# Optimization experiments

Hardware: AMD Instinct MI355X
Metric: run time of the kernel (lower is better)

## Reference

```python
import jax, jax.numpy as jnp
import numpy as np
from jax import lax


def _conv1d(x, w):
    # x: (B, L, C), w: (K, C, C), SAME padding (flax nnx.Conv default)
    return lax.conv_general_dilated(x, w, (1,), 'SAME', dimension_numbers=('NWC', 'WIO', 'NWC'))


def _message_passing(x, w, vertical, reverse):
    # x: (B, H, W, C). Sequential SCNN update along H (vertical) or W (horizontal):
    #   slice_i += relu(conv1d(slice_{i-1}))
    if not vertical:
        x = jnp.swapaxes(x, 1, 2)  # scan axis -> axis 1
    if reverse:
        x = x[:, ::-1]
    first = x[:, 0]                       # (B, Wd, C)
    rest = jnp.moveaxis(x[:, 1:], 1, 0)   # (L-1, B, Wd, C)

    def step(prev, row):
        new = row + jax.nn.relu(_conv1d(prev, w))
        return new, new

    _, out = lax.scan(step, first, rest)
    x = jnp.concatenate([first[:, None], jnp.moveaxis(out, 0, 1)], axis=1)
    if reverse:
        x = x[:, ::-1]
    if not vertical:
        x = jnp.swapaxes(x, 1, 2)
    return x


def _bn(x, scale, bias, eps=1e-5):
    # flax nnx.BatchNorm in training mode: batch stats over (B, H, W)
    mean = x.mean((0, 1, 2))
    var = x.var((0, 1, 2))
    return (x - mean) * lax.rsqrt(var + eps) * scale + bias


def reference(features, w_conv1, bn1_scale, bn1_bias, w_conv2, bn2_scale, bn2_bias,
              w_mp_vf, w_mp_vr, w_mp_hf, w_mp_hr, w_seg, b_seg,
              w_fc1, b_fc1, w_fc2, b_fc2):
    dn = ('NHWC', 'HWIO', 'NHWC')
    # dilated 3x3 conv (pad 4, dilation 4) -> BN -> relu
    x = lax.conv_general_dilated(features, w_conv1, (1, 1), [(4, 4), (4, 4)],
                                 rhs_dilation=(4, 4), dimension_numbers=dn)
    x = jax.nn.relu(_bn(x, bn1_scale, bn1_bias))
    # 1x1 conv -> BN -> relu
    x = lax.conv_general_dilated(x, w_conv2, (1, 1), 'SAME', dimension_numbers=dn)
    x = jax.nn.relu(_bn(x, bn2_scale, bn2_bias))
    # four SCNN message-passing directions (sequential scans)
    x = _message_passing(x, w_mp_vf, True, False)
    x = _message_passing(x, w_mp_vr, True, True)
    x = _message_passing(x, w_mp_hf, False, False)
    x = _message_passing(x, w_mp_hr, False, True)
    # seg head: dropout (deterministic -> identity) + 1x1 conv with bias
    x = lax.conv_general_dilated(x, w_seg, (1, 1), 'SAME', dimension_numbers=dn) + b_seg
    b, h, w, f = x.shape
    logits_seg = jax.image.resize(x, (b, h * 8, w * 8, f), method='linear')
    # existence head: softmax -> avg_pool 2x2 -> flatten -> MLP
    p = jax.nn.softmax(x, axis=-1)
    p = p.reshape(b, h // 2, 2, w // 2, 2, f).mean((2, 4))
    p = p.reshape(b, -1)  # (B, (h/2)*(w/2)*f) = (B, 4500)
    z = jax.nn.relu(p @ w_fc1 + b_fc1)
    logits_ext = z @ w_fc2 + b_fc2
    return logits_seg, logits_ext


def setup_inputs() -> dict:
    key = jax.random.key(0)
    ks = jax.random.split(key, 10)
    B, H, W, C = 16, 36, 100, 512
    n_lanes = 4
    s = 0.05
    return {
        'features': jax.random.normal(ks[0], (B, H, W, C), jnp.float32),
        'w_conv1': jax.random.normal(ks[1], (3, 3, 512, 1024), jnp.float32) * s,
        'bn1_scale': jnp.ones((1024,), jnp.float32),
        'bn1_bias': jnp.zeros((1024,), jnp.float32),
        'w_conv2': jax.random.normal(ks[2], (1, 1, 1024, 128), jnp.float32) * s,
        'bn2_scale': jnp.ones((128,), jnp.float32),
        'bn2_bias': jnp.zeros((128,), jnp.float32),
        'w_mp_vf': jax.random.normal(ks[3], (9, 128, 128), jnp.float32) * 0.02,
        'w_mp_vr': jax.random.normal(ks[4], (9, 128, 128), jnp.float32) * 0.02,
        'w_mp_hf': jax.random.normal(ks[5], (9, 128, 128), jnp.float32) * 0.02,
        'w_mp_hr': jax.random.normal(ks[6], (9, 128, 128), jnp.float32) * 0.02,
        'w_seg': jax.random.normal(ks[7], (1, 1, 128, n_lanes + 1), jnp.float32) * s,
        'b_seg': jnp.zeros((n_lanes + 1,), jnp.float32),
        'w_fc1': jax.random.normal(ks[8], (4500, 128), jnp.float32) * s,
        'b_fc1': jnp.zeros((128,), jnp.float32),
        'w_fc2': jax.random.normal(ks[9], (128, n_lanes), jnp.float32) * s,
        'b_fc2': jnp.zeros((n_lanes,), jnp.float32),
    }
```

## Files before the change

kernel.cpp:

```cpp
#include <hip/hip_runtime.h>
#include <hip/hip_bf16.h>

#define NB 16
#define NPOS 57600

typedef short bf16x8 __attribute__((ext_vector_type(8)));
typedef float f32x4 __attribute__((ext_vector_type(4)));

__device__ __forceinline__ float bf2f(unsigned short u) {
  union { unsigned int i; float f; } c; c.i = ((unsigned int)u) << 16; return c.f;
}
__device__ __forceinline__ unsigned short f2bf(float f) {
  union { float f; unsigned int i; } c; c.f = f;
  unsigned int x = c.i;
  x += 0x7fffu + ((x >> 16) & 1u);
  return (unsigned short)(x >> 16);
}
__device__ __forceinline__ unsigned int pk2(float lo, float hi) {
  return (unsigned int)f2bf(lo) | ((unsigned int)f2bf(hi) << 16);
}

__device__ __forceinline__ void gload_lds16(const void* g, void* l) {
  __builtin_amdgcn_global_load_lds(
      (const __attribute__((address_space(1))) unsigned int*)(g),
      (__attribute__((address_space(3))) unsigned int*)(l), 16, 0, 0);
}

__global__ __launch_bounds__(256) void convert_w1t(const float* __restrict__ w,
                                                   unsigned short* __restrict__ wt)
{
  int idx = blockIdx.x * 256 + threadIdx.x;
  int n = idx & 1023;
  int k0 = (idx >> 10) * 8;
  unsigned int o[4];
#pragma unroll
  for (int j = 0; j < 4; ++j) {
    float lo = w[(long)(k0 + 2*j)     * 1024 + n];
    float hi = w[(long)(k0 + 2*j + 1) * 1024 + n];
    o[j] = pk2(lo, hi);
  }
  *(uint4*)(wt + (long)n * 4608 + k0) = make_uint4(o[0], o[1], o[2], o[3]);
}

__global__ __launch_bounds__(256) void convert_w2t(const float* __restrict__ w,
                                                   unsigned short* __restrict__ wt)
{
  int idx = blockIdx.x * 256 + threadIdx.x;
  int n = idx & 127;
  int k0 = (idx >> 7) * 8;
  unsigned int o[4];
#pragma unroll
  for (int j = 0; j < 4; ++j) {
    float lo = w[(long)(k0 + 2*j)     * 128 + n];
    float hi = w[(long)(k0 + 2*j + 1) * 128 + n];
    o[j] = pk2(lo, hi);
  }
  *(uint4*)(wt + (long)n * 1024 + k0) = make_uint4(o[0], o[1], o[2], o[3]);
}

__global__ __launch_bounds__(256) void convert_wmp(const float* __restrict__ w,
                                                   unsigned short* __restrict__ wt)
{
  int idx = blockIdx.x * 256 + threadIdx.x;
  if (idx >= 18432) return;
  int co = idx & 127;
  int kg = idx >> 7;
  int k0 = kg * 8;
  int tap = k0 >> 7, ci0 = k0 & 127;
  const float* src = w + (long)tap * 16384 + (long)ci0 * 128 + co;
  unsigned int o[4];
#pragma unroll
  for (int j = 0; j < 4; ++j)
    o[j] = pk2(src[(2*j) * 128], src[(2*j+1) * 128]);
  *(uint4*)(wt + (long)co * 1152 + k0) = make_uint4(o[0], o[1], o[2], o[3]);
}

__global__ __launch_bounds__(256) void pad_features(const float* __restrict__ src,
                                                    unsigned short* __restrict__ dst)
{
  long idx = (long)blockIdx.x * 256 + threadIdx.x;
  if (idx >= 16L * 44 * 108 * 64) return;
  int c8 = (int)(idx & 63);
  long pos = idx >> 6;
  int wp = (int)(pos % 108); pos /= 108;
  int hp = (int)(pos % 44);
  int b  = (int)(pos / 44);
  uint4 o = make_uint4(0u, 0u, 0u, 0u);
  if (hp >= 4 && hp < 40 && wp >= 4 && wp < 104) {
    const float* s = src + (((long)b * 36 + (hp - 4)) * 100 + (wp - 4)) * 512 + c8 * 8;
    float4 v0 = *(const float4*)s;
    float4 v1 = *(const float4*)(s + 4);
    o = make_uint4(pk2(v0.x, v0.y), pk2(v0.z, v0.w), pk2(v1.x, v1.y), pk2(v1.z, v1.w));
  }
  *(uint4*)(dst + (((long)b * 44 + hp) * 108 + wp) * 512 + c8 * 8) = o;
}

__global__ __launch_bounds__(256) void conv1_mfma2(
    const unsigned short* __restrict__ inp,
    const unsigned short* __restrict__ w1t,
    unsigned short* __restrict__ x1)
{
  __shared__ unsigned short Al[128 * 32];
  __shared__ unsigned short Bl[128 * 32];
  const int tid  = threadIdx.x;
  const int lane = tid & 63;
  const int wave = tid >> 6;
  const int wm = wave >> 1, wn = wave & 1;
  const int bid  = blockIdx.x;
  const int nbid = (bid & 7) * 450 + (bid >> 3);
  const int n0 = (nbid & 7) * 128;
  const int m0 = (nbid >> 3) * 128;

  long aoff[2];
  const unsigned short* bsrc[2];
#pragma unroll
  for (int q = 0; q < 2; ++q) {
    int e = q * 256 + tid;
    int row = e >> 2;
    int kl  = (e & 3) * 8;
    int m = m0 + row;
    int w = m % 100, h = (m / 100) % 36, b = m / 3600;
    aoff[q] = (((long)b * 44 + h + 4) * 108 + (w + 4)) * 512 + kl;
    bsrc[q] = w1t + (long)(n0 + row) * 4608 + kl;
  }

  f32x4 acc[4][4];
#pragma unroll
  for (int i = 0; i < 4; ++i)
#pragma unroll
    for (int j = 0; j < 4; ++j) acc[i][j] = (f32x4){0.f, 0.f, 0.f, 0.f};

  const int fr = lane & 15;
  const int fk = (lane >> 4) * 8;
  const unsigned short* Alrd = Al + (wm * 64 + fr) * 32 + fk;
  const unsigned short* Blrd = Bl + (wn * 64 + fr) * 32 + fk;

  for (int k0 = 0; k0 < 4608; k0 += 32) {
    const int tap = k0 >> 9;
    const int ci0 = k0 & 511;
    const int dh = (tap / 3) * 4 - 4, dw = (tap % 3) * 4 - 4;
    const long delta = (long)(dh * 108 + dw) * 512 + ci0;
    __syncthreads();
#pragma unroll
    for (int q = 0; q < 2; ++q) {
      gload_lds16(inp + aoff[q] + delta, Al + (q * 256 + tid) * 8);
      gload_lds16(bsrc[q] + k0,          Bl + (q * 256 + tid) * 8);
    }
    __syncthreads();
    bf16x8 af[4], bfr[4];
#pragma unroll
    for (int m = 0; m < 4; ++m) af[m]  = *(const bf16x8*)(Alrd + m * 16 * 32);
#pragma unroll
    for (int n = 0; n < 4; ++n) bfr[n] = *(const bf16x8*)(Blrd + n * 16 * 32);
#pragma unroll
    for (int m = 0; m < 4; ++m)
#pragma unroll
      for (int n = 0; n < 4; ++n)
        acc[m][n] = __builtin_amdgcn_mfma_f32_16x16x32_bf16(af[m], bfr[n], acc[m][n], 0, 0, 0);
  }
  const int r0 = (lane >> 4) * 4;
#pragma unroll
  for (int m = 0; m < 4; ++m) {
    int row = m0 + wm * 64 + m * 16 + r0;
#pragma unroll
    for (int n = 0; n < 4; ++n) {
      int col = n0 + wn * 64 + n * 16 + fr;
#pragma unroll
      for (int j = 0; j < 4; ++j)
        x1[(long)(row + j) * 1024 + col] = f2bf(acc[m][n][j]);
    }
  }
}

__global__ __launch_bounds__(256) void conv1_mfma(
    const float* __restrict__ in,
    const unsigned short* __restrict__ w1t,
    unsigned short* __restrict__ x1)
{
  __shared__ unsigned short Al[128 * 32];
  __shared__ unsigned short Bl[128 * 32];
  const int tid  = threadIdx.x;
  const int lane = tid & 63;
  const int wave = tid >> 6;
  const int wm = wave >> 1, wn = wave & 1;
  const int m0 = blockIdx.y * 128;
  const int n0 = blockIdx.x * 128;

  int akl[2], ab_[2], ah_[2], aw_[2];
  const unsigned short* bsrc[2];
#pragma unroll
  for (int q = 0; q < 2; ++q) {
    int e = q * 256 + tid;
    int row = e >> 2;
    akl[q]  = (e & 3) * 8;
    int m = m0 + row;
    aw_[q] = m % 100;
    ah_[q] = (m / 100) % 36;
    ab_[q] = m / 3600;
    bsrc[q] = w1t + (long)(n0 + row) * 4608 + akl[q];
  }

  f32x4 acc[4][4];
#pragma unroll
  for (int i = 0; i < 4; ++i)
#pragma unroll
    for (int j = 0; j < 4; ++j) acc[i][j] = (f32x4){0.f, 0.f, 0.f, 0.f};

  const int fr = lane & 15;
  const int fk = (lane >> 4) * 8;
  const unsigned short* Alrd = Al + (wm * 64 + fr) * 32 + fk;
  const unsigned short* Blrd = Bl + (wn * 64 + fr) * 32 + fk;

  for (int k0 = 0; k0 < 4608; k0 += 32) {
    const int tap = k0 >> 9;
    const int ci0 = k0 & 511;
    const int dh = (tap / 3) * 4 - 4, dw = (tap % 3) * 4 - 4;
    unsigned int apk[2][4];
#pragma unroll
    for (int q = 0; q < 2; ++q) {
      int ih = ah_[q] + dh, iw = aw_[q] + dw;
      if ((unsigned)ih < 36u && (unsigned)iw < 100u) {
        const float* s = in + ((((long)ab_[q] * 36 + ih) * 100 + iw) << 9) + ci0 + akl[q];
        float4 v0 = *(const float4*)s;
        float4 v1 = *(const float4*)(s + 4);
        apk[q][0] = pk2(v0.x, v0.y); apk[q][1] = pk2(v0.z, v0.w);
        apk[q][2] = pk2(v1.x, v1.y); apk[q][3] = pk2(v1.z, v1.w);
      } else {
        apk[q][0] = apk[q][1] = apk[q][2] = apk[q][3] = 0u;
      }
    }
    __syncthreads();
#pragma unroll
    for (int q = 0; q < 2; ++q) {
      *(uint4*)(Al + (q * 256 + tid) * 8) = *(uint4*)apk[q];
      gload_lds16(bsrc[q] + k0, Bl + (q * 256 + tid) * 8);
    }
    __syncthreads();
    bf16x8 af[4], bfr[4];
#pragma unroll
    for (int m = 0; m < 4; ++m) af[m]  = *(const bf16x8*)(Alrd + m * 16 * 32);
#pragma unroll
    for (int n = 0; n < 4; ++n) bfr[n] = *(const bf16x8*)(Blrd + n * 16 * 32);
#pragma unroll
    for (int m = 0; m < 4; ++m)
#pragma unroll
      for (int n = 0; n < 4; ++n)
        acc[m][n] = __builtin_amdgcn_mfma_f32_16x16x32_bf16(af[m], bfr[n], acc[m][n], 0, 0, 0);
  }
  const int r0 = (lane >> 4) * 4;
#pragma unroll
  for (int m = 0; m < 4; ++m) {
    int row = m0 + wm * 64 + m * 16 + r0;
#pragma unroll
    for (int n = 0; n < 4; ++n) {
      int col = n0 + wn * 64 + n * 16 + fr;
#pragma unroll
      for (int j = 0; j < 4; ++j)
        x1[(long)(row + j) * 1024 + col] = f2bf(acc[m][n][j]);
    }
  }
}

__global__ __launch_bounds__(256) void gemm_mfma_128(
    const unsigned short* __restrict__ A,
    const unsigned short* __restrict__ Bt,
    float* __restrict__ C, int K)
{
  __shared__ unsigned short Al[128 * 32];
  __shared__ unsigned short Bl[128 * 32];
  const int tid  = threadIdx.x;
  const int lane = tid & 63;
  const int wave = tid >> 6;
  const int wm = wave >> 1, wn = wave & 1;
  const int m0 = blockIdx.x * 128;

  const unsigned short* asrc[2];
  const unsigned short* bsrc[2];
#pragma unroll
  for (int q = 0; q < 2; ++q) {
    int e = q * 256 + tid;
    int row = e >> 2;
    int kl  = (e & 3) * 8;
    asrc[q] = A  + (long)(m0 + row) * K + kl;
    bsrc[q] = Bt + (long)row * K + kl;
  }

  f32x4 acc[4][4];
#pragma unroll
  for (int i = 0; i < 4; ++i)
#pragma unroll
    for (int j = 0; j < 4; ++j) acc[i][j] = (f32x4){0.f, 0.f, 0.f, 0.f};

  const int fr = lane & 15;
  const int fk = (lane >> 4) * 8;
  const unsigned short* Alrd = Al + (wm * 64 + fr) * 32 + fk;
  const unsigned short* Blrd = Bl + (wn * 64 + fr) * 32 + fk;

  for (int k0 = 0; k0 < K; k0 += 32) {
    __syncthreads();
#pragma unroll
    for (int q = 0; q < 2; ++q) {
      gload_lds16(asrc[q] + k0, Al + (q * 256 + tid) * 8);
      gload_lds16(bsrc[q] + k0, Bl + (q * 256 + tid) * 8);
    }
    __syncthreads();
    bf16x8 af[4], bfr[4];
#pragma unroll
    for (int m = 0; m < 4; ++m) af[m]  = *(const bf16x8*)(Alrd + m * 16 * 32);
#pragma unroll
    for (int n = 0; n < 4; ++n) bfr[n] = *(const bf16x8*)(Blrd + n * 16 * 32);
#pragma unroll
    for (int m = 0; m < 4; ++m)
#pragma unroll
      for (int n = 0; n < 4; ++n)
        acc[m][n] = __builtin_amdgcn_mfma_f32_16x16x32_bf16(af[m], bfr[n], acc[m][n], 0, 0, 0);
  }
  const int r0 = (lane >> 4) * 4;
#pragma unroll
  for (int m = 0; m < 4; ++m) {
    int row = m0 + wm * 64 + m * 16 + r0;
#pragma unroll
    for (int n = 0; n < 4; ++n) {
      int col = wn * 64 + n * 16 + fr;
#pragma unroll
      for (int j = 0; j < 4; ++j)
        C[(long)(row + j) * 128 + col] = acc[m][n][j];
    }
  }
}

__global__ __launch_bounds__(256) void stats1(const unsigned short* __restrict__ x1,
                                              float* __restrict__ sum, float* __restrict__ ssq)
{
  const int tid = threadIdx.x;
  const int c0 = tid * 4;
  float s0=0,s1=0,s2=0,s3=0,q0=0,q1=0,q2=0,q3=0;
  for (int r = blockIdx.x; r < NPOS; r += gridDim.x) {
    uint2 v = *(const uint2*)(x1 + (long)r * 1024 + c0);
    float f0 = bf2f(v.x & 0xffffu), f1 = bf2f(v.x >> 16);
    float f2 = bf2f(v.y & 0xffffu), f3 = bf2f(v.y >> 16);
    s0 += f0; q0 += f0*f0;  s1 += f1; q1 += f1*f1;
    s2 += f2; q2 += f2*f2;  s3 += f3; q3 += f3*f3;
  }
  atomicAdd(&sum[c0+0], s0); atomicAdd(&ssq[c0+0], q0);
  atomicAdd(&sum[c0+1], s1); atomicAdd(&ssq[c0+1], q1);
  atomicAdd(&sum[c0+2], s2); atomicAdd(&ssq[c0+2], q2);
  atomicAdd(&sum[c0+3], s3); atomicAdd(&ssq[c0+3], q3);
}

__global__ void finalize_bn(const float* __restrict__ sum, const float* __restrict__ ssq,
                            const float* __restrict__ scale, const float* __restrict__ bias,
                            float* __restrict__ ab, int C, float invN)
{
  int c = blockIdx.x * blockDim.x + threadIdx.x;
  if (c >= C) return;
  float mean = sum[c] * invN;
  float var  = ssq[c] * invN - mean * mean;
  float a = scale[c] * rsqrtf(var + 1e-5f);
  ab[c] = a;
  ab[C + c] = bias[c] - mean * a;
}

__global__ __launch_bounds__(256) void bnrelu_x1(unsigned short* __restrict__ x1,
                                                 const float* __restrict__ ab)
{
  long base = ((long)blockIdx.x * 256 + threadIdx.x) * 8;
  int c0 = (int)(base & 1023);
  uint4 v = *(uint4*)(x1 + base);
  unsigned int w[4] = {v.x, v.y, v.z, v.w};
  unsigned int o[4];
#pragma unroll
  for (int j = 0; j < 4; ++j) {
    int c = c0 + j * 2;
    float lo = bf2f((unsigned short)(w[j] & 0xffffu));
    float hi = bf2f((unsigned short)(w[j] >> 16));
    lo = fmaxf(fmaf(lo, ab[c],     ab[1024 + c]),     0.f);
    hi = fmaxf(fmaf(hi, ab[c + 1], ab[1024 + c + 1]), 0.f);
    o[j] = pk2(lo, hi);
  }
  *(uint4*)(x1 + base) = make_uint4(o[0], o[1], o[2], o[3]);
}

__global__ __launch_bounds__(256) void stats2(const float* __restrict__ x2,
                                              float* __restrict__ sum, float* __restrict__ ssq)
{
  const int c = threadIdx.x & 127;
  const int g = threadIdx.x >> 7;
  float s = 0.f, q = 0.f;
  for (int r = blockIdx.x * 2 + g; r < NPOS; r += gridDim.x * 2) {
    float v = x2[(long)r * 128 + c];
    s += v; q += v * v;
  }
  atomicAdd(&sum[c], s); atomicAdd(&ssq[c], q);
}

__global__ __launch_bounds__(256) void apply_bn(float* __restrict__ x, const float* __restrict__ ab)
{
  int idx = (blockIdx.x * 256 + threadIdx.x) * 4;
  if (idx >= NPOS * 128) return;
  int c = idx & 127;
  float4 v = *(float4*)(x + idx);
  v.x = fmaxf(fmaf(v.x, ab[c+0], ab[128+c+0]), 0.f);
  v.y = fmaxf(fmaf(v.y, ab[c+1], ab[128+c+1]), 0.f);
  v.z = fmaxf(fmaf(v.z, ab[c+2], ab[128+c+2]), 0.f);
  v.w = fmaxf(fmaf(v.w, ab[c+3], ab[128+c+3]), 0.f);
  *(float4*)(x + idx) = v;
}

#define MPROWS 120
#define MPBUF (MPROWS * 128)
template<int MT, int MH>
__global__ __launch_bounds__(512, 2) void mp_fused2(
    float* __restrict__ x2, const unsigned short* __restrict__ wt,
    const int L, const int posStride, const int rowStride,
    const int i0, const int di, const int nsteps)
{
  __shared__ unsigned short rowbuf[2 * MPBUF];
  __shared__ float xch[MT * 8 * 16 * 17];
  const int tid  = threadIdx.x;
  const int lane = tid & 63;
  const int wave = tid >> 6;
  const int ng   = wave & 3;
  const int kh   = wave >> 2;
  const int fr   = lane & 15;
  const int ks   = lane >> 4;
  float* xb = x2 + (long)blockIdx.x * 460800;

  for (int i = tid; i < (2 * MPBUF) / 8; i += 512)
    *(uint4*)(rowbuf + i * 8) = make_uint4(0u, 0u, 0u, 0u);

  const unsigned short* wb = wt + (long)(ng * 32 + fr) * 1152 + kh * 576 + ks * 8;
  bf16x8 bfrag[2][18];
#pragma unroll
  for (int nt = 0; nt < 2; ++nt)
#pragma unroll
    for (int kk = 0; kk < 18; ++kk)
      bfrag[nt][kk] = *(const bf16x8*)(wb + nt * 16 * 1152 + kk * 32);

  __syncthreads();
  for (int e = tid * 4; e < L * 128; e += 2048) {
    int w = e >> 7, c = e & 127;
    float4 v = *(const float4*)(xb + (long)i0 * rowStride + (long)w * posStride + c);
    int br = w + 4;
    int byte = (br * 256 + c * 2) ^ ((br & 7) << 4);
    *(uint2*)((char*)rowbuf + byte) = make_uint2(pk2(v.x, v.y), pk2(v.z, v.w));
  }
  __syncthreads();

#define MP_EPI(mt)                                                             \
  _Pragma("unroll")                                                            \
  for (int nt = 0; nt < 2; ++nt) {                                             \
    const int col = ng * 32 + nt * 16 + fr;                                    \
    const float* src = &xch[(((mt) * 8 + ng * 2 + nt) * 16) * 17];             \
    _Pragma("unroll")                                                          \
    for (int j = 0; j < 4; ++j) {                                              \
      const int m = (mt) * 16 + ks * 4 + j;                                    \
      if (m < L) {                                                             \
        float v = acc[mt][nt][j] + src[(ks * 4 + j) * 17 + fr];                \
        long off = (long)i * rowStride + (long)m * posStride + col;            \
        float nv = xb[off] + fmaxf(v, 0.f);                                    \
        xb[off] = nv;                                                          \
        int br = m + 4;                                                        \
        int byte = (br * 256 + col * 2) ^ ((br & 7) << 4);                     \
        *(unsigned short*)(nxtb + byte) = f2bf(nv);                            \
      }                                                                        \
    }                                                                          \
  }

  for (int s = 1; s <= nsteps; ++s) {
    const char* curb = (const char*)rowbuf + (((s & 1) ^ 1) * MPBUF) * 2;
    char* nxtb = (char*)rowbuf + ((s & 1) * MPBUF) * 2;
    const int i = i0 + s * di;

    f32x4 acc[MT][2];
#pragma unroll
    for (int mt = 0; mt < MT; ++mt) {
      acc[mt][0] = (f32x4){0.f, 0.f, 0.f, 0.f};
      acc[mt][1] = (f32x4){0.f, 0.f, 0.f, 0.f};
    }

#pragma unroll
    for (int kk = 0; kk < 18; ++kk) {
      const int k0 = kh * 576 + kk * 32;
      const int tap = k0 >> 7;
      const int colb = ((k0 & 127) + ks * 8) * 2;
      const int br0 = fr + tap;
      const int byte0 = (br0 * 256 + colb) ^ ((br0 & 7) << 4);
#pragma unroll
      for (int mt = 0; mt < MT; ++mt) {
        bf16x8 af = *(const bf16x8*)(curb + byte0 + mt * 4096);
        acc[mt][0] = __builtin_amdgcn_mfma_f32_16x16x32_bf16(af, bfrag[0][kk], acc[mt][0], 0, 0, 0);
        acc[mt][1] = __builtin_amdgcn_mfma_f32_16x16x32_bf16(af, bfrag[1][kk], acc[mt][1], 0, 0, 0);
      }
    }

    if (kh == 0) {
#pragma unroll
      for (int mt = MH; mt < MT; ++mt) {
#pragma unroll
        for (int nt = 0; nt < 2; ++nt) {
          float* dst = &xch[((mt * 8 + ng * 2 + nt) * 16) * 17];
#pragma unroll
          for (int j = 0; j < 4; ++j)
            dst[(ks * 4 + j) * 17 + fr] = acc[mt][nt][j];
        }
      }
    } else {
#pragma unroll
      for (int mt = 0; mt < MH; ++mt) {
#pragma unroll
        for (int nt = 0; nt < 2; ++nt) {
          float* dst = &xch[((mt * 8 + ng * 2 + nt) * 16) * 17];
#pragma unroll
          for (int j = 0; j < 4; ++j)
            dst[(ks * 4 + j) * 17 + fr] = acc[mt][nt][j];
        }
      }
    }
    __syncthreads();
    if (kh == 0) {
#pragma unroll
      for (int mt = 0; mt < MH; ++mt) { MP_EPI(mt) }
    } else {
#pragma unroll
      for (int mt = MH; mt < MT; ++mt) { MP_EPI(mt) }
    }
    __syncthreads();
  }
#undef MP_EPI
}

__global__ __launch_bounds__(256) void seg_head(
    const float* __restrict__ xn, const float* __restrict__ w_seg,
    const float* __restrict__ b_seg, float* __restrict__ logits)
{
  __shared__ float ws[128 * 5];
  __shared__ float xs[32][129];
  const int tid = threadIdx.x;
  for (int i = tid; i < 640; i += 256) ws[i] = w_seg[i];
  const int pos0 = blockIdx.x * 32;
  for (int idx = tid; idx < 32 * 32; idx += 256) {
    int r = idx >> 5, q = idx & 31;
    float4 v = *(const float4*)(xn + (long)(pos0 + r) * 128 + q * 4);
    xs[r][q*4+0]=v.x; xs[r][q*4+1]=v.y; xs[r][q*4+2]=v.z; xs[r][q*4+3]=v.w;
  }
  __syncthreads();
  int r = tid >> 3, f = tid & 7;
  if (f < 5) {
    float acc = b_seg[f];
#pragma unroll 4
    for (int ci = 0; ci < 128; ++ci) acc = fmaf(xs[r][ci], ws[ci*5 + f], acc);
    logits[(long)(pos0 + r) * 5 + f] = acc;
  }
}

__global__ __launch_bounds__(256) void softpool(const float* __restrict__ logits, float* __restrict__ p)
{
  int idx = blockIdx.x * 256 + threadIdx.x;
  if (idx >= 16 * 18 * 50) return;
  int ww = idx % 50, hh = (idx / 50) % 18, b = idx / 900;
  float avg[5] = {0,0,0,0,0};
#pragma unroll
  for (int i = 0; i < 2; ++i)
#pragma unroll
    for (int j = 0; j < 2; ++j) {
      const float* L = logits + ((long)((b*36 + hh*2 + i) * 100) + ww*2 + j) * 5;
      float l0=L[0], l1=L[1], l2=L[2], l3=L[3], l4=L[4];
      float m = fmaxf(fmaxf(fmaxf(l0,l1), fmaxf(l2,l3)), l4);
      float e0=expf(l0-m), e1=expf(l1-m), e2=expf(l2-m), e3=expf(l3-m), e4=expf(l4-m);
      float inv = 1.f / (e0+e1+e2+e3+e4);
      avg[0] += e0*inv; avg[1] += e1*inv; avg[2] += e2*inv; avg[3] += e3*inv; avg[4] += e4*inv;
    }
  float* dst = p + (long)b * 4500 + (hh * 50 + ww) * 5;
#pragma unroll
  for (int f = 0; f < 5; ++f) dst[f] = avg[f] * 0.25f;
}

__global__ __launch_bounds__(128) void fc1_kernel(
    const float* __restrict__ p, const float* __restrict__ w,
    const float* __restrict__ bias, float* __restrict__ z)
{
  __shared__ float ps[4500];
  const int b = blockIdx.x, tid = threadIdx.x;
  for (int i = tid; i < 4500; i += 128) ps[i] = p[(long)b * 4500 + i];
  __syncthreads();
  float acc = bias[tid];
#pragma unroll 4
  for (int m = 0; m < 4500; ++m) acc = fmaf(ps[m], w[(long)m * 128 + tid], acc);
  z[b * 128 + tid] = fmaxf(acc, 0.f);
}

__global__ void fc2_kernel(const float* __restrict__ z, const float* __restrict__ w,
                           const float* __restrict__ bias, float* __restrict__ out)
{
  int t = threadIdx.x;
  if (t >= 64) return;
  int b = t >> 2, j = t & 3;
  float acc = bias[j];
#pragma unroll 4
  for (int n = 0; n < 128; ++n) acc = fmaf(z[b*128 + n], w[n*4 + j], acc);
  out[b*4 + j] = acc;
}

__global__ __launch_bounds__(256) void resize_bilinear(
    const float* __restrict__ logits, float* __restrict__ out)
{
  int idx = blockIdx.x * 256 + threadIdx.x;
  if (idx >= 18432000) return;
  int f = idx % 5;
  int t = idx / 5;
  int ow = t % 800; t /= 800;
  int oh = t % 288;
  int b = t / 288;
  float sh = (oh + 0.5f) * 0.125f - 0.5f;
  float sw = (ow + 0.5f) * 0.125f - 0.5f;
  int h0 = (int)floorf(sh); float fh = sh - (float)h0;
  int w0 = (int)floorf(sw); float fw = sw - (float)w0;
  int h1 = min(h0 + 1, 35); h0 = max(h0, 0);
  int w1 = min(w0 + 1, 99); w0 = max(w0, 0);
  const float* Lb = logits + (long)b * 36 * 100 * 5 + f;
  float v00 = Lb[(h0*100 + w0)*5], v01 = Lb[(h0*100 + w1)*5];
  float v10 = Lb[(h1*100 + w0)*5], v11 = Lb[(h1*100 + w1)*5];
  float v = (1.f-fh) * ((1.f-fw)*v00 + fw*v01) + fh * ((1.f-fw)*v10 + fw*v11);
  out[idx] = v;
}

extern "C" void kernel_launch(void* const* d_in, const int* in_sizes, int n_in,
                              void* d_out, int out_size, void* d_ws, size_t ws_size,
                              hipStream_t stream)
{
  (void)in_sizes; (void)n_in; (void)out_size;
  const float* features = (const float*)d_in[0];
  const float* w_conv1  = (const float*)d_in[1];
  const float* bn1_s    = (const float*)d_in[2];
  const float* bn1_b    = (const float*)d_in[3];
  const float* w_conv2  = (const float*)d_in[4];
  const float* bn2_s    = (const float*)d_in[5];
  const float* bn2_b    = (const float*)d_in[6];
  const float* w_vf     = (const float*)d_in[7];
  const float* w_vr     = (const float*)d_in[8];
  const float* w_hf     = (const float*)d_in[9];
  const float* w_hr     = (const float*)d_in[10];
  const float* w_seg    = (const float*)d_in[11];
  const float* b_seg    = (const float*)d_in[12];
  const float* w_fc1    = (const float*)d_in[13];
  const float* b_fc1    = (const float*)d_in[14];
  const float* w_fc2    = (const float*)d_in[15];
  const float* b_fc2    = (const float*)d_in[16];

  char* ws = (char*)d_ws;
  unsigned short* x1  = (unsigned short*)ws;
  unsigned short* w1t = (unsigned short*)(ws + 117964800);
  float* x2     = (float*)(ws + 117964800);
  float* logits = (float*)(ws + 147456000);
  unsigned short* wtmp = (unsigned short*)(ws + 147456000);
  float* pbuf   = (float*)(ws + 148608000);
  float* zbuf   = (float*)(ws + 148896000);
  float* stats  = (float*)(ws + 148904192);
  float* ab1    = (float*)(ws + 148913408);
  float* ab2    = (float*)(ws + 148921600);
  unsigned short* w2t = (unsigned short*)(ws + 148922624);
  unsigned short* in_pad = (unsigned short*)(ws + 149184768);
  const bool use_pad = ws_size >= 227041536ULL;
  float* outf   = (float*)d_out;

  hipMemsetAsync(stats, 0, 2304 * sizeof(float), stream);
  convert_w1t<<<2304, 256, 0, stream>>>(w_conv1, w1t);
  convert_w2t<<<64, 256, 0, stream>>>(w_conv2, w2t);
  convert_wmp<<<72, 256, 0, stream>>>(w_vf, wtmp + 0 * 147456);
  convert_wmp<<<72, 256, 0, stream>>>(w_vr, wtmp + 1 * 147456);
  convert_wmp<<<72, 256, 0, stream>>>(w_hf, wtmp + 2 * 147456);
  convert_wmp<<<72, 256, 0, stream>>>(w_hr, wtmp + 3 * 147456);

  if (use_pad) {
    pad_features<<<19008, 256, 0, stream>>>(features, in_pad);
    conv1_mfma2<<<3600, 256, 0, stream>>>(in_pad, w1t, x1);
  } else {
    conv1_mfma<<<dim3(8, 450), 256, 0, stream>>>(features, w1t, x1);
  }
  stats1<<<512, 256, 0, stream>>>(x1, stats, stats + 1024);
  finalize_bn<<<4, 256, 0, stream>>>(stats, stats + 1024, bn1_s, bn1_b, ab1, 1024, 1.0f/57600.0f);
  bnrelu_x1<<<28800, 256, 0, stream>>>(x1, ab1);
  gemm_mfma_128<<<450, 256, 0, stream>>>(x1, w2t, x2, 1024);
  stats2<<<256, 256, 0, stream>>>(x2, stats + 2048, stats + 2176);
  finalize_bn<<<1, 128, 0, stream>>>(stats + 2048, stats + 2176, bn2_s, bn2_b, ab2, 128, 1.0f/57600.0f);
  apply_bn<<<7200, 256, 0, stream>>>(x2, ab2);

  mp_fused2<7,3><<<NB, 512, 0, stream>>>(x2, wtmp + 0 * 147456, 100, 128,   12800, 0,  +1, 35);
  mp_fused2<7,3><<<NB, 512, 0, stream>>>(x2, wtmp + 1 * 147456, 100, 128,   12800, 35, -1, 35);
  mp_fused2<3,1><<<NB, 512, 0, stream>>>(x2, wtmp + 2 * 147456, 36,  12800, 128,   0,  +1, 99);
  mp_fused2<3,1><<<NB, 512, 0, stream>>>(x2, wtmp + 3 * 147456, 36,  12800, 128,   99, -1, 99);

  seg_head<<<1800, 256, 0, stream>>>(x2, w_seg, b_seg, logits);
  softpool<<<57, 256, 0, stream>>>(logits, pbuf);
  fc1_kernel<<<16, 128, 0, stream>>>(pbuf, w_fc1, b_fc1, zbuf);
  fc2_kernel<<<1, 64, 0, stream>>>(zbuf, w_fc2, b_fc2, outf + 18432000);
  resize_bilinear<<<72000, 256, 0, stream>>>(logits, outf);
}
```

Baseline: 3.555 ms.

## Split message-passing rows across two wave groups with 1024-thread blocks

The sequential SCNN message-passing kernel now runs 16 waves per block instead of 8, with a new wave-group index splitting the row tiles between two groups. Each wave computes fewer M tiles per step, so the serial per-step chain gets shorter. The weight fragments are no longer held in registers across steps; they are reloaded from global memory (likely cache hits) inside the K loop, which cuts register pressure so 1024 threads fit. The cost is repeated weight loads every step, and the kh==0 waves still do the whole epilogue while the kh==1 waves only write partial sums.

```diff
diff --git a/kernel.cpp b/kernel.cpp
--- a/kernel.cpp
+++ b/kernel.cpp
@@ -409,36 +409,30 @@
 
 #define MPROWS 120
 #define MPBUF (MPROWS * 128)
-template<int MT, int MH>
-__global__ __launch_bounds__(512, 2) void mp_fused2(
+template<int MT, int MTL0>
+__global__ __launch_bounds__(1024) void mp_fused8(
     float* __restrict__ x2, const unsigned short* __restrict__ wt,
     const int L, const int posStride, const int rowStride,
     const int i0, const int di, const int nsteps)
 {
+  constexpr int MTL1 = MT - MTL0;
+  constexpr int NMT  = (MTL0 > MTL1) ? MTL0 : MTL1;
   __shared__ unsigned short rowbuf[2 * MPBUF];
-  __shared__ float xch[MT * 8 * 16 * 17];
+  __shared__ float xch[MT * 4 * 2 * 16 * 17];
   const int tid  = threadIdx.x;
   const int lane = tid & 63;
   const int wave = tid >> 6;
   const int ng   = wave & 3;
-  const int kh   = wave >> 2;
+  const int kh   = (wave >> 2) & 1;
+  const int mg   = wave >> 3;
   const int fr   = lane & 15;
   const int ks   = lane >> 4;
   float* xb = x2 + (long)blockIdx.x * 460800;
 
-  for (int i = tid; i < (2 * MPBUF) / 8; i += 512)
+  for (int i = tid; i < (2 * MPBUF) / 8; i += 1024)
     *(uint4*)(rowbuf + i * 8) = make_uint4(0u, 0u, 0u, 0u);
-
-  const unsigned short* wb = wt + (long)(ng * 32 + fr) * 1152 + kh * 576 + ks * 8;
-  bf16x8 bfrag[2][18];
-#pragma unroll
-  for (int nt = 0; nt < 2; ++nt)
-#pragma unroll
-    for (int kk = 0; kk < 18; ++kk)
-      bfrag[nt][kk] = *(const bf16x8*)(wb + nt * 16 * 1152 + kk * 32);
-
   __syncthreads();
-  for (int e = tid * 4; e < L * 128; e += 2048) {
+  for (int e = tid * 4; e < L * 128; e += 4096) {
     int w = e >> 7, c = e & 127;
     float4 v = *(const float4*)(xb + (long)i0 * rowStride + (long)w * posStride + c);
     int br = w + 4;
@@ -447,16 +441,19 @@
   }
   __syncthreads();
 
-#define MP_EPI(mt)                                                             \
+  const unsigned short* wb = wt + (long)(ng * 32 + fr) * 1152 + kh * 576 + ks * 8;
+
+#define XCH(mtg, nt, r) xch[((((mtg) * 4 + ng) * 2 + (nt)) * 16 + (r)) * 17 + fr]
+
+#define MP_EPI(mtg, pi)                                                        \
   _Pragma("unroll")                                                            \
   for (int nt = 0; nt < 2; ++nt) {                                             \
     const int col = ng * 32 + nt * 16 + fr;                                    \
-    const float* src = &xch[(((mt) * 8 + ng * 2 + nt) * 16) * 17];             \
     _Pragma("unroll")                                                          \
     for (int j = 0; j < 4; ++j) {                                              \
-      const int m = (mt) * 16 + ks * 4 + j;                                    \
+      const int m = (mtg) * 16 + ks * 4 + j;                                   \
       if (m < L) {                                                             \
-        float v = acc[mt][nt][j] + src[(ks * 4 + j) * 17 + fr];                \
+        float v = acc[pi][nt][j] + XCH(mtg, nt, ks * 4 + j);                   \
         long off = (long)i * rowStride + (long)m * posStride + col;            \
         float nv = xb[off] + fmaxf(v, 0.f);                                    \
         xb[off] = nv;                                                          \
@@ -472,9 +469,9 @@
     char* nxtb = (char*)rowbuf + ((s & 1) * MPBUF) * 2;
     const int i = i0 + s * di;
 
-    f32x4 acc[MT][2];
-#pragma unroll
-    for (int mt = 0; mt < MT; ++mt) {
+    f32x4 acc[NMT][2];
+#pragma unroll
+    for (int mt = 0; mt < NMT; ++mt) {
       acc[mt][0] = (f32x4){0.f, 0.f, 0.f, 0.f};
       acc[mt][1] = (f32x4){0.f, 0.f, 0.f, 0.f};
     }
@@ -484,50 +481,60 @@
       const int k0 = kh * 576 + kk * 32;
       const int tap = k0 >> 7;
       const int colb = ((k0 & 127) + ks * 8) * 2;
+      bf16x8 bf0 = *(const bf16x8*)(wb + kk * 32);
+      bf16x8 bf1 = *(const bf16x8*)(wb + 16 * 1152 + kk * 32);
       const int br0 = fr + tap;
       const int byte0 = (br0 * 256 + colb) ^ ((br0 & 7) << 4);
-#pragma unroll
-      for (int mt = 0; mt < MT; ++mt) {
-        bf16x8 af = *(const bf16x8*)(curb + byte0 + mt * 4096);
-        acc[mt][0] = __builtin_amdgcn_mfma_f32_16x16x32_bf16(af, bfrag[0][kk], acc[mt][0], 0, 0, 0);
-        acc[mt][1] = __builtin_amdgcn_mfma_f32_16x16x32_bf16(af, bfrag[1][kk], acc[mt][1], 0, 0, 0);
-      }
-    }
-
-    if (kh == 0) {
-#pragma unroll
-      for (int mt = MH; mt < MT; ++mt) {
-#pragma unroll
-        for (int nt = 0; nt < 2; ++nt) {
-          float* dst = &xch[((mt * 8 + ng * 2 + nt) * 16) * 17];
-#pragma unroll
-          for (int j = 0; j < 4; ++j)
-            dst[(ks * 4 + j) * 17 + fr] = acc[mt][nt][j];
+      if (mg == 0) {
+#pragma unroll
+        for (int mt = 0; mt < MTL0; ++mt) {
+          bf16x8 af = *(const bf16x8*)(curb + byte0 + mt * 4096);
+          acc[mt][0] = __builtin_amdgcn_mfma_f32_16x16x32_bf16(af, bf0, acc[mt][0], 0, 0, 0);
+          acc[mt][1] = __builtin_amdgcn_mfma_f32_16x16x32_bf16(af, bf1, acc[mt][1], 0, 0, 0);
+        }
+      } else {
+#pragma unroll
+        for (int mt = 0; mt < MTL1; ++mt) {
+          bf16x8 af = *(const bf16x8*)(curb + byte0 + (MTL0 + mt) * 4096);
+          acc[mt][0] = __builtin_amdgcn_mfma_f32_16x16x32_bf16(af, bf0, acc[mt][0], 0, 0, 0);
+          acc[mt][1] = __builtin_amdgcn_mfma_f32_16x16x32_bf16(af, bf1, acc[mt][1], 0, 0, 0);
         }
       }
-    } else {
-#pragma unroll
-      for (int mt = 0; mt < MH; ++mt) {
-#pragma unroll
-        for (int nt = 0; nt < 2; ++nt) {
-          float* dst = &xch[((mt * 8 + ng * 2 + nt) * 16) * 17];
-#pragma unroll
-          for (int j = 0; j < 4; ++j)
-            dst[(ks * 4 + j) * 17 + fr] = acc[mt][nt][j];
-        }
+    }
+
+    if (kh == 1) {
+      if (mg == 0) {
+#pragma unroll
+        for (int mt = 0; mt < MTL0; ++mt)
+#pragma unroll
+          for (int nt = 0; nt < 2; ++nt)
+#pragma unroll
+            for (int j = 0; j < 4; ++j)
+              XCH(mt, nt, ks * 4 + j) = acc[mt][nt][j];
+      } else {
+#pragma unroll
+        for (int mt = 0; mt < MTL1; ++mt)
+#pragma unroll
+          for (int nt = 0; nt < 2; ++nt)
+#pragma unroll
+            for (int j = 0; j < 4; ++j)
+              XCH(MTL0 + mt, nt, ks * 4 + j) = acc[mt][nt][j];
       }
     }
     __syncthreads();
     if (kh == 0) {
-#pragma unroll
-      for (int mt = 0; mt < MH; ++mt) { MP_EPI(mt) }
-    } else {
-#pragma unroll
-      for (int mt = MH; mt < MT; ++mt) { MP_EPI(mt) }
+      if (mg == 0) {
+#pragma unroll
+        for (int mt = 0; mt < MTL0; ++mt) { MP_EPI(mt, mt) }
+      } else {
+#pragma unroll
+        for (int mt = 0; mt < MTL1; ++mt) { MP_EPI(MTL0 + mt, mt) }
+      }
     }
     __syncthreads();
   }
 #undef MP_EPI
+#undef XCH
 }
 
 __global__ __launch_bounds__(256) void seg_head(
@@ -686,10 +693,10 @@
   finalize_bn<<<1, 128, 0, stream>>>(stats + 2048, stats + 2176, bn2_s, bn2_b, ab2, 128, 1.0f/57600.0f);
   apply_bn<<<7200, 256, 0, stream>>>(x2, ab2);
 
-  mp_fused2<7,3><<<NB, 512, 0, stream>>>(x2, wtmp + 0 * 147456, 100, 128,   12800, 0,  +1, 35);
-  mp_fused2<7,3><<<NB, 512, 0, stream>>>(x2, wtmp + 1 * 147456, 100, 128,   12800, 35, -1, 35);
-  mp_fused2<3,1><<<NB, 512, 0, stream>>>(x2, wtmp + 2 * 147456, 36,  12800, 128,   0,  +1, 99);
-  mp_fused2<3,1><<<NB, 512, 0, stream>>>(x2, wtmp + 3 * 147456, 36,  12800, 128,   99, -1, 99);
+  mp_fused8<7,4><<<NB, 1024, 0, stream>>>(x2, wtmp + 0 * 147456, 100, 128,   12800, 0,  +1, 35);
+  mp_fused8<7,4><<<NB, 1024, 0, stream>>>(x2, wtmp + 1 * 147456, 100, 128,   12800, 35, -1, 35);
+  mp_fused8<3,2><<<NB, 1024, 0, stream>>>(x2, wtmp + 2 * 147456, 36,  12800, 128,   0,  +1, 99);
+  mp_fused8<3,2><<<NB, 1024, 0, stream>>>(x2, wtmp + 3 * 147456, 36,  12800, 128,   99, -1, 99);
 
   seg_head<<<1800, 256, 0, stream>>>(x2, w_seg, b_seg, logits);
   softpool<<<57, 256, 0, stream>>>(logits, pbuf);
```

Measured after the change: 6.159 ms. +73.2%, slower.
